# Kernel tuning notes

Measured on AMD Instinct MI355X. Metric: run time of the kernel, lower is better.

The kernel has to match this reference:

```python
import jax, jax.numpy as jnp
import numpy as np

BATCH, D_INNER, DT_RANK, N = 256, 5120, 160, 16

def _softplus_thresh(z, threshold=20.0):
    # softplus(z) with beta=1; linear above threshold (matches ttnn.softplus(parameter1=1, parameter2=20))
    return jnp.where(z > threshold, z, jax.nn.softplus(z))

def setup_inputs() -> dict:
    key = jax.random.key(0)
    ks = jax.random.split(key, 9)
    s = lambda d: 1.0 / np.sqrt(d)
    return {
        "x": jax.random.normal(ks[0], (1, 1, BATCH, D_INNER), jnp.float32),
        "h": jax.random.normal(ks[1], (BATCH, D_INNER, N), jnp.float32) * 0.1,
        "W_delta": jax.random.normal(ks[2], (D_INNER, DT_RANK), jnp.float32) * s(D_INNER),
        "W_dt": jax.random.normal(ks[3], (DT_RANK, D_INNER), jnp.float32) * s(DT_RANK),
        "b_dt": jax.random.normal(ks[4], (D_INNER,), jnp.float32) * 0.1,
        "A_log": jax.random.uniform(ks[5], (D_INNER, N), jnp.float32, 0.0, 1.5),
        "W_B": jax.random.normal(ks[6], (D_INNER, N), jnp.float32) * s(D_INNER),
        "W_C": jax.random.normal(ks[7], (D_INNER, N), jnp.float32) * s(D_INNER),
        "D": jax.random.normal(ks[8], (D_INNER,), jnp.float32),
    }

def reference(x, h, W_delta, W_dt, b_dt, A_log, W_B, W_C, D):
    # x: (1,1,B,d_inner) single decode step; h: (B,d_inner,n) SSM state
    xb = x.reshape(BATCH, D_INNER)                           # (B, d)
    # delta = softplus(x @ W_delta @ W_dt + b_dt)           -> (B, d)
    dt = _softplus_thresh((xb @ W_delta) @ W_dt + b_dt)
    A = -jnp.exp(A_log)                                      # (d, n)
    abar = jnp.exp(dt[:, :, None] * A[None, :, :])           # (B, d, n)
    Bp = xb @ W_B                                            # (B, n)
    # bbar * x: delta * B * x, broadcast over state dim
    bx = (dt * xb)[:, :, None] * Bp[:, None, :]              # (B, d, n)
    h_new = abar * h + bx                                    # (B, d, n) new hidden state
    C = xb @ W_C                                             # (B, n)
    y = jnp.einsum("bdn,bn->bd", h_new, C) + xb * D          # readout + skip (D)
    return y.reshape(1, 1, BATCH, D_INNER)
```

## Files before the change

### kernel.cpp

```cpp
#include <hip/hip_runtime.h>
#include <math.h>

#define BATCH 256
#define DIN   5120
#define RANK  160
#define NS    16
#define NCAT  192

__global__ __launch_bounds__(256) void k1_gemm(
    const float* __restrict__ x, const float* __restrict__ Wd,
    const float* __restrict__ WB, const float* __restrict__ WC,
    float* __restrict__ P, float* __restrict__ Bp, float* __restrict__ Cc)
{
    __shared__ float xT[32][64];
    __shared__ float Wt[32][64];
    const int t  = threadIdx.x;
    const int m0 = blockIdx.x * 64;
    const int n0 = blockIdx.y * 64;
    const int k0 = blockIdx.z * 128;
    const int tm = (t >> 4) * 4;
    const int tn = (t & 15) * 4;

    const int lm  = t >> 2;
    const int lk  = (t & 3) * 8;
    const int ln  = t & 63;
    const int lkb = (t >> 6) * 8;

    const float* wsrc; int wstr;
    {
        const int c = n0 + ln;
        if (c < RANK)            { wsrc = Wd + c;                wstr = RANK; }
        else if (c < RANK + NS)  { wsrc = WB + (c - RANK);       wstr = NS;   }
        else                     { wsrc = WC + (c - RANK - NS);  wstr = NS;   }
    }

    float acc[4][4] = {{0.f}};

    for (int ks = 0; ks < 4; ++ks) {
        const int kb = k0 + ks * 32;
        {
            const float* src = x + (size_t)(m0 + lm) * DIN + kb + lk;
            const float4 a0 = *(const float4*)src;
            const float4 a1 = *(const float4*)(src + 4);
            xT[lk+0][lm]=a0.x; xT[lk+1][lm]=a0.y; xT[lk+2][lm]=a0.z; xT[lk+3][lm]=a0.w;
            xT[lk+4][lm]=a1.x; xT[lk+5][lm]=a1.y; xT[lk+6][lm]=a1.z; xT[lk+7][lm]=a1.w;
        }
        {
            const float* wp = wsrc + (size_t)(kb + lkb) * wstr;
            #pragma unroll
            for (int i = 0; i < 8; ++i) { Wt[lkb + i][ln] = *wp; wp += wstr; }
        }
        __syncthreads();
        #pragma unroll
        for (int k = 0; k < 32; ++k) {
            const float4 a = *(const float4*)&xT[k][tm];
            const float4 b = *(const float4*)&Wt[k][tn];
            acc[0][0] += a.x*b.x; acc[0][1] += a.x*b.y; acc[0][2] += a.x*b.z; acc[0][3] += a.x*b.w;
            acc[1][0] += a.y*b.x; acc[1][1] += a.y*b.y; acc[1][2] += a.y*b.z; acc[1][3] += a.y*b.w;
            acc[2][0] += a.z*b.x; acc[2][1] += a.z*b.y; acc[2][2] += a.z*b.z; acc[2][3] += a.z*b.w;
            acc[3][0] += a.w*b.x; acc[3][1] += a.w*b.y; acc[3][2] += a.w*b.z; acc[3][3] += a.w*b.w;
        }
        __syncthreads();
    }

    #pragma unroll
    for (int i = 0; i < 4; ++i) {
        const int gm = m0 + tm + i;
        #pragma unroll
        for (int j = 0; j < 4; ++j) {
            const int c = n0 + tn + j;
            float* dst;
            if (c < RANK)           dst = P  + gm * RANK + c;
            else if (c < RANK + NS) dst = Bp + gm * NS + (c - RANK);
            else                    dst = Cc + gm * NS + (c - RANK - NS);
            atomicAdd(dst, acc[i][j]);
        }
    }
}

__device__ __forceinline__ float softplus20(float z)
{
    if (z > 20.f) return z;
    return fmaxf(z, 0.f) + log1pf(__expf(-fabsf(z)));
}

__global__ __launch_bounds__(256) void k2a_gemm(
    const float* __restrict__ P, const float* __restrict__ Wdt,
    const float* __restrict__ bdt, float* __restrict__ dtb)
{
    __shared__ float aT[32][64];
    __shared__ float Bt[32][64];
    const int t  = threadIdx.x;
    const int m0 = blockIdx.x * 64;
    const int n0 = blockIdx.y * 64;
    const int tm = (t >> 4) * 4;
    const int tn = (t & 15) * 4;

    const int lm  = t >> 2;
    const int lk  = (t & 3) * 8;
    const int ln  = t & 63;
    const int lkb = (t >> 6) * 8;

    float acc[4][4] = {{0.f}};

    for (int ks = 0; ks < 5; ++ks) {
        const int kb = ks * 32;
        {
            const float* src = P + (size_t)(m0 + lm) * RANK + kb + lk;
            const float4 a0 = *(const float4*)src;
            const float4 a1 = *(const float4*)(src + 4);
            aT[lk+0][lm]=a0.x; aT[lk+1][lm]=a0.y; aT[lk+2][lm]=a0.z; aT[lk+3][lm]=a0.w;
            aT[lk+4][lm]=a1.x; aT[lk+5][lm]=a1.y; aT[lk+6][lm]=a1.z; aT[lk+7][lm]=a1.w;
        }
        {
            const float* wp = Wdt + (size_t)(kb + lkb) * DIN + n0 + ln;
            #pragma unroll
            for (int i = 0; i < 8; ++i) { Bt[lkb + i][ln] = wp[(size_t)i * DIN]; }
        }
        __syncthreads();
        #pragma unroll
        for (int k = 0; k < 32; ++k) {
            const float4 a = *(const float4*)&aT[k][tm];
            const float4 b = *(const float4*)&Bt[k][tn];
            acc[0][0] += a.x*b.x; acc[0][1] += a.x*b.y; acc[0][2] += a.x*b.z; acc[0][3] += a.x*b.w;
            acc[1][0] += a.y*b.x; acc[1][1] += a.y*b.y; acc[1][2] += a.y*b.z; acc[1][3] += a.y*b.w;
            acc[2][0] += a.z*b.x; acc[2][1] += a.z*b.y; acc[2][2] += a.z*b.z; acc[2][3] += a.z*b.w;
            acc[3][0] += a.w*b.x; acc[3][1] += a.w*b.y; acc[3][2] += a.w*b.z; acc[3][3] += a.w*b.w;
        }
        __syncthreads();
    }

    const float4 bz = *(const float4*)&bdt[n0 + tn];
    #pragma unroll
    for (int i = 0; i < 4; ++i) {
        const int gm = m0 + tm + i;
        float4 o;
        o.x = softplus20(acc[i][0] + bz.x);
        o.y = softplus20(acc[i][1] + bz.y);
        o.z = softplus20(acc[i][2] + bz.z);
        o.w = softplus20(acc[i][3] + bz.w);
        *(float4*)&dtb[(size_t)gm * DIN + n0 + tn] = o;
    }
}

__global__ __launch_bounds__(256) void k2b_ssm(
    const float* __restrict__ dtb, const float* __restrict__ x,
    const float* __restrict__ h, const float* __restrict__ A_log,
    const float* __restrict__ Bp, const float* __restrict__ Cc,
    const float* __restrict__ Dv, float* __restrict__ y)
{
    __shared__ float sB[4][NS];
    __shared__ float sC[4][NS];

    const int tid = threadIdx.x;
    const int d   = blockIdx.x * 256 + tid;
    const int b0  = blockIdx.y * 4;

    if (tid < 64)                    sB[tid >> 4][tid & 15] = Bp[b0 * NS + tid];
    else if (tid < 128) { int u = tid - 64; sC[u >> 4][u & 15] = Cc[b0 * NS + u]; }
    __syncthreads();

    float A2[NS];
    {
        const float4* ap = (const float4*)(A_log + (size_t)d * NS);
        #pragma unroll
        for (int q = 0; q < 4; ++q) {
            const float4 a4 = ap[q];
            A2[4*q+0] = -1.442695041f * __expf(a4.x);
            A2[4*q+1] = -1.442695041f * __expf(a4.y);
            A2[4*q+2] = -1.442695041f * __expf(a4.z);
            A2[4*q+3] = -1.442695041f * __expf(a4.w);
        }
    }
    const float dv = Dv[d];

    #pragma unroll
    for (int b = 0; b < 4; ++b) {
        const int gb = b0 + b;
        const float dtv = dtb[(size_t)gb * DIN + d];
        const float xv  = x[(size_t)gb * DIN + d];
        const float dtx = dtv * xv;
        const float4* hp = (const float4*)(h + ((size_t)gb * DIN + d) * NS);
        float s = 0.f;
        #pragma unroll
        for (int q = 0; q < 4; ++q) {
            const float4 h4 = hp[q];
            s += (exp2f(dtv * A2[4*q+0]) * h4.x + dtx * sB[b][4*q+0]) * sC[b][4*q+0];
            s += (exp2f(dtv * A2[4*q+1]) * h4.y + dtx * sB[b][4*q+1]) * sC[b][4*q+1];
            s += (exp2f(dtv * A2[4*q+2]) * h4.z + dtx * sB[b][4*q+2]) * sC[b][4*q+2];
            s += (exp2f(dtv * A2[4*q+3]) * h4.w + dtx * sB[b][4*q+3]) * sC[b][4*q+3];
        }
        y[(size_t)gb * DIN + d] = s + xv * dv;
    }
}

extern "C" void kernel_launch(void* const* d_in, const int* in_sizes, int n_in,
                              void* d_out, int out_size, void* d_ws, size_t ws_size,
                              hipStream_t stream)
{
    const float* x     = (const float*)d_in[0];
    const float* h     = (const float*)d_in[1];
    const float* Wd    = (const float*)d_in[2];
    const float* Wdt   = (const float*)d_in[3];
    const float* bdt   = (const float*)d_in[4];
    const float* A_log = (const float*)d_in[5];
    const float* WB    = (const float*)d_in[6];
    const float* WC    = (const float*)d_in[7];
    const float* Dv    = (const float*)d_in[8];
    float* out = (float*)d_out;

    float* ws  = (float*)d_ws;
    float* P   = ws;
    float* Bp  = ws + BATCH * RANK;
    float* Cc  = Bp + BATCH * NS;
    float* dtb = Cc + BATCH * NS;

    hipMemsetAsync(ws, 0, (size_t)BATCH * NCAT * sizeof(float), stream);

    k1_gemm <<<dim3(4, 3, 40), 256, 0, stream>>>(x, Wd, WB, WC, P, Bp, Cc);
    k2a_gemm<<<dim3(4, 80),    256, 0, stream>>>(P, Wdt, bdt, dtb);
    k2b_ssm <<<dim3(20, 64),   256, 0, stream>>>(dtb, x, h, A_log, Bp, Cc, Dv, out);
}
```

Measured before the change: 205.4 us.

## Fuse three kernels into one persistent kernel with software grid barriers

Merges the x-projection GEMM, the dt GEMM with softplus, and the SSM readout into one kernel launched with 480 blocks, separated by atomic-counter grid barriers. The SSM phase becomes a grid-stride loop over the original 1280 tiles. The intent is to remove the launch gaps and tail effects between the three kernels. It relies on all 480 blocks being co-resident, otherwise the spin barriers deadlock. The barriers themselves add spin-wait cost, and fewer blocks in the memory-bound SSM phase may lower achieved bandwidth.

```diff
diff --git a/kernel.cpp b/kernel.cpp
--- a/kernel.cpp
+++ b/kernel.cpp
@@ -6,76 +6,17 @@
 #define RANK  160
 #define NS    16
 #define NCAT  192
-
-__global__ __launch_bounds__(256) void k1_gemm(
-    const float* __restrict__ x, const float* __restrict__ Wd,
-    const float* __restrict__ WB, const float* __restrict__ WC,
-    float* __restrict__ P, float* __restrict__ Bp, float* __restrict__ Cc)
-{
-    __shared__ float xT[32][64];
-    __shared__ float Wt[32][64];
-    const int t  = threadIdx.x;
-    const int m0 = blockIdx.x * 64;
-    const int n0 = blockIdx.y * 64;
-    const int k0 = blockIdx.z * 128;
-    const int tm = (t >> 4) * 4;
-    const int tn = (t & 15) * 4;
-
-    const int lm  = t >> 2;
-    const int lk  = (t & 3) * 8;
-    const int ln  = t & 63;
-    const int lkb = (t >> 6) * 8;
-
-    const float* wsrc; int wstr;
-    {
-        const int c = n0 + ln;
-        if (c < RANK)            { wsrc = Wd + c;                wstr = RANK; }
-        else if (c < RANK + NS)  { wsrc = WB + (c - RANK);       wstr = NS;   }
-        else                     { wsrc = WC + (c - RANK - NS);  wstr = NS;   }
-    }
-
-    float acc[4][4] = {{0.f}};
-
-    for (int ks = 0; ks < 4; ++ks) {
-        const int kb = k0 + ks * 32;
-        {
-            const float* src = x + (size_t)(m0 + lm) * DIN + kb + lk;
-            const float4 a0 = *(const float4*)src;
-            const float4 a1 = *(const float4*)(src + 4);
-            xT[lk+0][lm]=a0.x; xT[lk+1][lm]=a0.y; xT[lk+2][lm]=a0.z; xT[lk+3][lm]=a0.w;
-            xT[lk+4][lm]=a1.x; xT[lk+5][lm]=a1.y; xT[lk+6][lm]=a1.z; xT[lk+7][lm]=a1.w;
-        }
-        {
-            const float* wp = wsrc + (size_t)(kb + lkb) * wstr;
-            #pragma unroll
-            for (int i = 0; i < 8; ++i) { Wt[lkb + i][ln] = *wp; wp += wstr; }
-        }
-        __syncthreads();
-        #pragma unroll
-        for (int k = 0; k < 32; ++k) {
-            const float4 a = *(const float4*)&xT[k][tm];
-            const float4 b = *(const float4*)&Wt[k][tn];
-            acc[0][0] += a.x*b.x; acc[0][1] += a.x*b.y; acc[0][2] += a.x*b.z; acc[0][3] += a.x*b.w;
-            acc[1][0] += a.y*b.x; acc[1][1] += a.y*b.y; acc[1][2] += a.y*b.z; acc[1][3] += a.y*b.w;
-            acc[2][0] += a.z*b.x; acc[2][1] += a.z*b.y; acc[2][2] += a.z*b.z; acc[2][3] += a.z*b.w;
-            acc[3][0] += a.w*b.x; acc[3][1] += a.w*b.y; acc[3][2] += a.w*b.z; acc[3][3] += a.w*b.w;
-        }
-        __syncthreads();
-    }
-
-    #pragma unroll
-    for (int i = 0; i < 4; ++i) {
-        const int gm = m0 + tm + i;
-        #pragma unroll
-        for (int j = 0; j < 4; ++j) {
-            const int c = n0 + tn + j;
-            float* dst;
-            if (c < RANK)           dst = P  + gm * RANK + c;
-            else if (c < RANK + NS) dst = Bp + gm * NS + (c - RANK);
-            else                    dst = Cc + gm * NS + (c - RANK - NS);
-            atomicAdd(dst, acc[i][j]);
-        }
-    }
+#define GRID  480
+
+__device__ __forceinline__ void grid_barrier(int* ctr, int nblk)
+{
+    __syncthreads();
+    if (threadIdx.x == 0) {
+        __hip_atomic_fetch_add(ctr, 1, __ATOMIC_RELEASE, __HIP_MEMORY_SCOPE_AGENT);
+        while (__hip_atomic_load(ctr, __ATOMIC_ACQUIRE, __HIP_MEMORY_SCOPE_AGENT) < nblk)
+            __builtin_amdgcn_s_sleep(2);
+    }
+    __syncthreads();
 }
 
 __device__ __forceinline__ float softplus20(float z)
@@ -84,113 +25,184 @@
     return fmaxf(z, 0.f) + log1pf(__expf(-fabsf(z)));
 }
 
-__global__ __launch_bounds__(256) void k2a_gemm(
-    const float* __restrict__ P, const float* __restrict__ Wdt,
-    const float* __restrict__ bdt, float* __restrict__ dtb)
-{
-    __shared__ float aT[32][64];
-    __shared__ float Bt[32][64];
-    const int t  = threadIdx.x;
-    const int m0 = blockIdx.x * 64;
-    const int n0 = blockIdx.y * 64;
-    const int tm = (t >> 4) * 4;
-    const int tn = (t & 15) * 4;
-
-    const int lm  = t >> 2;
-    const int lk  = (t & 3) * 8;
-    const int ln  = t & 63;
-    const int lkb = (t >> 6) * 8;
-
-    float acc[4][4] = {{0.f}};
-
-    for (int ks = 0; ks < 5; ++ks) {
-        const int kb = ks * 32;
+__global__ __launch_bounds__(256) void mega(
+    const float* __restrict__ x, const float* __restrict__ h,
+    const float* __restrict__ Wd, const float* __restrict__ Wdt,
+    const float* __restrict__ bdt, const float* __restrict__ A_log,
+    const float* __restrict__ WB, const float* __restrict__ WC,
+    const float* __restrict__ Dv,
+    int* __restrict__ bar, float* __restrict__ P,
+    float* __restrict__ Bp, float* __restrict__ Cc,
+    float* __restrict__ dtb, float* __restrict__ y)
+{
+    __shared__ float sA[32][64];
+    __shared__ float sW[32][64];
+    __shared__ float sB4[4][NS];
+    __shared__ float sC4[4][NS];
+
+    const int t   = threadIdx.x;
+    const int blk = blockIdx.x;
+
+    {
+        const int m0 = (blk & 3) * 64;
+        const int n0 = ((blk >> 2) % 3) * 64;
+        const int k0 = (blk / 12) * 128;
+        const int tm = (t >> 4) * 4;
+        const int tn = (t & 15) * 4;
+        const int lm  = t >> 2;
+        const int lk  = (t & 3) * 8;
+        const int ln  = t & 63;
+        const int lkb = (t >> 6) * 8;
+
+        const float* wsrc; int wstr;
         {
-            const float* src = P + (size_t)(m0 + lm) * RANK + kb + lk;
-            const float4 a0 = *(const float4*)src;
-            const float4 a1 = *(const float4*)(src + 4);
-            aT[lk+0][lm]=a0.x; aT[lk+1][lm]=a0.y; aT[lk+2][lm]=a0.z; aT[lk+3][lm]=a0.w;
-            aT[lk+4][lm]=a1.x; aT[lk+5][lm]=a1.y; aT[lk+6][lm]=a1.z; aT[lk+7][lm]=a1.w;
-        }
+            const int c = n0 + ln;
+            if (c < RANK)            { wsrc = Wd + c;                wstr = RANK; }
+            else if (c < RANK + NS)  { wsrc = WB + (c - RANK);       wstr = NS;   }
+            else                     { wsrc = WC + (c - RANK - NS);  wstr = NS;   }
+        }
+
+        float acc[4][4] = {{0.f}};
+
+        for (int ks = 0; ks < 4; ++ks) {
+            const int kb = k0 + ks * 32;
+            {
+                const float* src = x + (size_t)(m0 + lm) * DIN + kb + lk;
+                const float4 a0 = *(const float4*)src;
+                const float4 a1 = *(const float4*)(src + 4);
+                sA[lk+0][lm]=a0.x; sA[lk+1][lm]=a0.y; sA[lk+2][lm]=a0.z; sA[lk+3][lm]=a0.w;
+                sA[lk+4][lm]=a1.x; sA[lk+5][lm]=a1.y; sA[lk+6][lm]=a1.z; sA[lk+7][lm]=a1.w;
+            }
+            {
+                const float* wp = wsrc + (size_t)(kb + lkb) * wstr;
+                #pragma unroll
+                for (int i = 0; i < 8; ++i) { sW[lkb + i][ln] = *wp; wp += wstr; }
+            }
+            __syncthreads();
+            #pragma unroll
+            for (int k = 0; k < 32; ++k) {
+                const float4 a = *(const float4*)&sA[k][tm];
+                const float4 b = *(const float4*)&sW[k][tn];
+                acc[0][0] += a.x*b.x; acc[0][1] += a.x*b.y; acc[0][2] += a.x*b.z; acc[0][3] += a.x*b.w;
+                acc[1][0] += a.y*b.x; acc[1][1] += a.y*b.y; acc[1][2] += a.y*b.z; acc[1][3] += a.y*b.w;
+                acc[2][0] += a.z*b.x; acc[2][1] += a.z*b.y; acc[2][2] += a.z*b.z; acc[2][3] += a.z*b.w;
+                acc[3][0] += a.w*b.x; acc[3][1] += a.w*b.y; acc[3][2] += a.w*b.z; acc[3][3] += a.w*b.w;
+            }
+            __syncthreads();
+        }
+
+        #pragma unroll
+        for (int i = 0; i < 4; ++i) {
+            const int gm = m0 + tm + i;
+            #pragma unroll
+            for (int j = 0; j < 4; ++j) {
+                const int c = n0 + tn + j;
+                float* dst;
+                if (c < RANK)           dst = P  + gm * RANK + c;
+                else if (c < RANK + NS) dst = Bp + gm * NS + (c - RANK);
+                else                    dst = Cc + gm * NS + (c - RANK - NS);
+                atomicAdd(dst, acc[i][j]);
+            }
+        }
+    }
+
+    grid_barrier(&bar[0], GRID);
+
+    if (blk < 320) {
+        const int m0 = (blk & 3) * 64;
+        const int n0 = (blk >> 2) * 64;
+        const int tm = (t >> 4) * 4;
+        const int tn = (t & 15) * 4;
+        const int lm  = t >> 2;
+        const int lk  = (t & 3) * 8;
+        const int ln  = t & 63;
+        const int lkb = (t >> 6) * 8;
+
+        float acc[4][4] = {{0.f}};
+
+        for (int ks = 0; ks < 5; ++ks) {
+            const int kb = ks * 32;
+            {
+                const float* src = P + (size_t)(m0 + lm) * RANK + kb + lk;
+                const float4 a0 = *(const float4*)src;
+                const float4 a1 = *(const float4*)(src + 4);
+                sA[lk+0][lm]=a0.x; sA[lk+1][lm]=a0.y; sA[lk+2][lm]=a0.z; sA[lk+3][lm]=a0.w;
+                sA[lk+4][lm]=a1.x; sA[lk+5][lm]=a1.y; sA[lk+6][lm]=a1.z; sA[lk+7][lm]=a1.w;
+            }
+            {
+                const float* wp = Wdt + (size_t)(kb + lkb) * DIN + n0 + ln;
+                #pragma unroll
+                for (int i = 0; i < 8; ++i) { sW[lkb + i][ln] = wp[(size_t)i * DIN]; }
+            }
+            __syncthreads();
+            #pragma unroll
+            for (int k = 0; k < 32; ++k) {
+                const float4 a = *(const float4*)&sA[k][tm];
+                const float4 b = *(const float4*)&sW[k][tn];
+                acc[0][0] += a.x*b.x; acc[0][1] += a.x*b.y; acc[0][2] += a.x*b.z; acc[0][3] += a.x*b.w;
+                acc[1][0] += a.y*b.x; acc[1][1] += a.y*b.y; acc[1][2] += a.y*b.z; acc[1][3] += a.y*b.w;
+                acc[2][0] += a.z*b.x; acc[2][1] += a.z*b.y; acc[2][2] += a.z*b.z; acc[2][3] += a.z*b.w;
+                acc[3][0] += a.w*b.x; acc[3][1] += a.w*b.y; acc[3][2] += a.w*b.z; acc[3][3] += a.w*b.w;
+            }
+            __syncthreads();
+        }
+
+        const float4 bz = *(const float4*)&bdt[n0 + tn];
+        #pragma unroll
+        for (int i = 0; i < 4; ++i) {
+            const int gm = m0 + tm + i;
+            float4 o;
+            o.x = softplus20(acc[i][0] + bz.x);
+            o.y = softplus20(acc[i][1] + bz.y);
+            o.z = softplus20(acc[i][2] + bz.z);
+            o.w = softplus20(acc[i][3] + bz.w);
+            *(float4*)&dtb[(size_t)gm * DIN + n0 + tn] = o;
+        }
+    }
+
+    grid_barrier(&bar[1], GRID);
+
+    for (int vb = blk; vb < 1280; vb += GRID) {
+        const int d  = (vb % 20) * 256 + t;
+        const int b0 = (vb / 20) * 4;
+
+        __syncthreads();
+        if (t < 64)                    sB4[t >> 4][t & 15] = Bp[b0 * NS + t];
+        else if (t < 128) { int u = t - 64; sC4[u >> 4][u & 15] = Cc[b0 * NS + u]; }
+        __syncthreads();
+
+        float A2[NS];
         {
-            const float* wp = Wdt + (size_t)(kb + lkb) * DIN + n0 + ln;
-            #pragma unroll
-            for (int i = 0; i < 8; ++i) { Bt[lkb + i][ln] = wp[(size_t)i * DIN]; }
-        }
-        __syncthreads();
+            const float4* ap = (const float4*)(A_log + (size_t)d * NS);
+            #pragma unroll
+            for (int q = 0; q < 4; ++q) {
+                const float4 a4 = ap[q];
+                A2[4*q+0] = -1.442695041f * __expf(a4.x);
+                A2[4*q+1] = -1.442695041f * __expf(a4.y);
+                A2[4*q+2] = -1.442695041f * __expf(a4.z);
+                A2[4*q+3] = -1.442695041f * __expf(a4.w);
+            }
+        }
+        const float dv = Dv[d];
+
         #pragma unroll
-        for (int k = 0; k < 32; ++k) {
-            const float4 a = *(const float4*)&aT[k][tm];
-            const float4 b = *(const float4*)&Bt[k][tn];
-            acc[0][0] += a.x*b.x; acc[0][1] += a.x*b.y; acc[0][2] += a.x*b.z; acc[0][3] += a.x*b.w;
-            acc[1][0] += a.y*b.x; acc[1][1] += a.y*b.y; acc[1][2] += a.y*b.z; acc[1][3] += a.y*b.w;
-            acc[2][0] += a.z*b.x; acc[2][1] += a.z*b.y; acc[2][2] += a.z*b.z; acc[2][3] += a.z*b.w;
-            acc[3][0] += a.w*b.x; acc[3][1] += a.w*b.y; acc[3][2] += a.w*b.z; acc[3][3] += a.w*b.w;
-        }
-        __syncthreads();
-    }
-
-    const float4 bz = *(const float4*)&bdt[n0 + tn];
-    #pragma unroll
-    for (int i = 0; i < 4; ++i) {
-        const int gm = m0 + tm + i;
-        float4 o;
-        o.x = softplus20(acc[i][0] + bz.x);
-        o.y = softplus20(acc[i][1] + bz.y);
-        o.z = softplus20(acc[i][2] + bz.z);
-        o.w = softplus20(acc[i][3] + bz.w);
-        *(float4*)&dtb[(size_t)gm * DIN + n0 + tn] = o;
-    }
-}
-
-__global__ __launch_bounds__(256) void k2b_ssm(
-    const float* __restrict__ dtb, const float* __restrict__ x,
-    const float* __restrict__ h, const float* __restrict__ A_log,
-    const float* __restrict__ Bp, const float* __restrict__ Cc,
-    const float* __restrict__ Dv, float* __restrict__ y)
-{
-    __shared__ float sB[4][NS];
-    __shared__ float sC[4][NS];
-
-    const int tid = threadIdx.x;
-    const int d   = blockIdx.x * 256 + tid;
-    const int b0  = blockIdx.y * 4;
-
-    if (tid < 64)                    sB[tid >> 4][tid & 15] = Bp[b0 * NS + tid];
-    else if (tid < 128) { int u = tid - 64; sC[u >> 4][u & 15] = Cc[b0 * NS + u]; }
-    __syncthreads();
-
-    float A2[NS];
-    {
-        const float4* ap = (const float4*)(A_log + (size_t)d * NS);
-        #pragma unroll
-        for (int q = 0; q < 4; ++q) {
-            const float4 a4 = ap[q];
-            A2[4*q+0] = -1.442695041f * __expf(a4.x);
-            A2[4*q+1] = -1.442695041f * __expf(a4.y);
-            A2[4*q+2] = -1.442695041f * __expf(a4.z);
-            A2[4*q+3] = -1.442695041f * __expf(a4.w);
-        }
-    }
-    const float dv = Dv[d];
-
-    #pragma unroll
-    for (int b = 0; b < 4; ++b) {
-        const int gb = b0 + b;
-        const float dtv = dtb[(size_t)gb * DIN + d];
-        const float xv  = x[(size_t)gb * DIN + d];
-        const float dtx = dtv * xv;
-        const float4* hp = (const float4*)(h + ((size_t)gb * DIN + d) * NS);
-        float s = 0.f;
-        #pragma unroll
-        for (int q = 0; q < 4; ++q) {
-            const float4 h4 = hp[q];
-            s += (exp2f(dtv * A2[4*q+0]) * h4.x + dtx * sB[b][4*q+0]) * sC[b][4*q+0];
-            s += (exp2f(dtv * A2[4*q+1]) * h4.y + dtx * sB[b][4*q+1]) * sC[b][4*q+1];
-            s += (exp2f(dtv * A2[4*q+2]) * h4.z + dtx * sB[b][4*q+2]) * sC[b][4*q+2];
-            s += (exp2f(dtv * A2[4*q+3]) * h4.w + dtx * sB[b][4*q+3]) * sC[b][4*q+3];
-        }
-        y[(size_t)gb * DIN + d] = s + xv * dv;
+        for (int b = 0; b < 4; ++b) {
+            const int gb = b0 + b;
+            const float dtv = dtb[(size_t)gb * DIN + d];
+            const float xv  = x[(size_t)gb * DIN + d];
+            const float dtx = dtv * xv;
+            const float4* hp = (const float4*)(h + ((size_t)gb * DIN + d) * NS);
+            float s = 0.f;
+            #pragma unroll
+            for (int q = 0; q < 4; ++q) {
+                const float4 h4 = hp[q];
+                s += (exp2f(dtv * A2[4*q+0]) * h4.x + dtx * sB4[b][4*q+0]) * sC4[b][4*q+0];
+                s += (exp2f(dtv * A2[4*q+1]) * h4.y + dtx * sB4[b][4*q+1]) * sC4[b][4*q+1];
+                s += (exp2f(dtv * A2[4*q+2]) * h4.z + dtx * sB4[b][4*q+2]) * sC4[b][4*q+2];
+                s += (exp2f(dtv * A2[4*q+3]) * h4.w + dtx * sB4[b][4*q+3]) * sC4[b][4*q+3];
+            }
+            y[(size_t)gb * DIN + d] = s + xv * dv;
+        }
     }
 }
 
@@ -209,15 +221,14 @@
     const float* Dv    = (const float*)d_in[8];
     float* out = (float*)d_out;
 
-    float* ws  = (float*)d_ws;
-    float* P   = ws;
-    float* Bp  = ws + BATCH * RANK;
+    int*   bar = (int*)d_ws;
+    float* P   = (float*)d_ws + 16;
+    float* Bp  = P  + BATCH * RANK;
     float* Cc  = Bp + BATCH * NS;
     float* dtb = Cc + BATCH * NS;
 
-    hipMemsetAsync(ws, 0, (size_t)BATCH * NCAT * sizeof(float), stream);
-
-    k1_gemm <<<dim3(4, 3, 40), 256, 0, stream>>>(x, Wd, WB, WC, P, Bp, Cc);
-    k2a_gemm<<<dim3(4, 80),    256, 0, stream>>>(P, Wdt, bdt, dtb);
-    k2b_ssm <<<dim3(20, 64),   256, 0, stream>>>(dtb, x, h, A_log, Bp, Cc, Dv, out);
-}
+    hipMemsetAsync(d_ws, 0, (16 + (size_t)BATCH * NCAT) * sizeof(float), stream);
+
+    mega<<<dim3(GRID), 256, 0, stream>>>(x, h, Wd, Wdt, bdt, A_log, WB, WC, Dv,
+                                         bar, P, Bp, Cc, dtb, out);
+}
```

Result: slower. 301.0 us (+46.5%).

## Replace split-K atomics with partial-sum reduce and coalesce SSM state reads

Applied to the files above, without the earlier changes.

The first GEMM now writes per-split partial sums to a workspace buffer, and a separate reduce kernel sums them, replacing the memset plus scalar atomicAdds. The SSM kernel is restructured so each group of 4 lanes reads one contiguous 64-byte row of h with float4 loads and combines the results with wave shuffles, giving coalesced access to the large state tensor. In exchange it adds one kernel launch and about 7.8 MB of partial-sum traffic, and it recomputes exp(A_log) for every batch row instead of reusing it across 4.

```diff
diff --git a/kernel.cpp b/kernel.cpp
--- a/kernel.cpp
+++ b/kernel.cpp
@@ -6,18 +6,20 @@
 #define RANK  160
 #define NS    16
 #define NCAT  192
-
-__global__ __launch_bounds__(256) void k1_gemm(
+#define NSPLIT 40
+
+__global__ __launch_bounds__(256) void k1a_gemm(
     const float* __restrict__ x, const float* __restrict__ Wd,
     const float* __restrict__ WB, const float* __restrict__ WC,
-    float* __restrict__ P, float* __restrict__ Bp, float* __restrict__ Cc)
+    float* __restrict__ psum)
 {
     __shared__ float xT[32][64];
     __shared__ float Wt[32][64];
     const int t  = threadIdx.x;
     const int m0 = blockIdx.x * 64;
     const int n0 = blockIdx.y * 64;
-    const int k0 = blockIdx.z * 128;
+    const int z  = blockIdx.z;
+    const int k0 = z * 128;
     const int tm = (t >> 4) * 4;
     const int tn = (t & 15) * 4;
 
@@ -63,19 +65,28 @@
         __syncthreads();
     }
 
+    float* dst = psum + (size_t)z * (BATCH * NCAT);
     #pragma unroll
     for (int i = 0; i < 4; ++i) {
         const int gm = m0 + tm + i;
-        #pragma unroll
-        for (int j = 0; j < 4; ++j) {
-            const int c = n0 + tn + j;
-            float* dst;
-            if (c < RANK)           dst = P  + gm * RANK + c;
-            else if (c < RANK + NS) dst = Bp + gm * NS + (c - RANK);
-            else                    dst = Cc + gm * NS + (c - RANK - NS);
-            atomicAdd(dst, acc[i][j]);
-        }
-    }
+        float4 o; o.x = acc[i][0]; o.y = acc[i][1]; o.z = acc[i][2]; o.w = acc[i][3];
+        *(float4*)&dst[(size_t)gm * NCAT + n0 + tn] = o;
+    }
+}
+
+__global__ __launch_bounds__(256) void k1r_reduce(
+    const float* __restrict__ psum, float* __restrict__ P,
+    float* __restrict__ Bp, float* __restrict__ Cc)
+{
+    const int o = blockIdx.x * 256 + threadIdx.x;
+    float s = 0.f;
+    #pragma unroll 8
+    for (int z = 0; z < NSPLIT; ++z) s += psum[(size_t)z * (BATCH * NCAT) + o];
+    const int gm = o / NCAT;
+    const int gc = o - gm * NCAT;
+    if (gc < RANK)           P [gm * RANK + gc]             = s;
+    else if (gc < RANK + NS) Bp[gm * NS   + gc - RANK]      = s;
+    else                     Cc[gm * NS   + gc - RANK - NS] = s;
 }
 
 __device__ __forceinline__ float softplus20(float z)
@@ -143,54 +154,51 @@
     }
 }
 
-__global__ __launch_bounds__(256) void k2b_ssm(
+__global__ __launch_bounds__(256) void k3_ssm(
     const float* __restrict__ dtb, const float* __restrict__ x,
     const float* __restrict__ h, const float* __restrict__ A_log,
     const float* __restrict__ Bp, const float* __restrict__ Cc,
     const float* __restrict__ Dv, float* __restrict__ y)
 {
-    __shared__ float sB[4][NS];
-    __shared__ float sC[4][NS];
-
-    const int tid = threadIdx.x;
-    const int d   = blockIdx.x * 256 + tid;
-    const int b0  = blockIdx.y * 4;
-
-    if (tid < 64)                    sB[tid >> 4][tid & 15] = Bp[b0 * NS + tid];
-    else if (tid < 128) { int u = tid - 64; sC[u >> 4][u & 15] = Cc[b0 * NS + u]; }
-    __syncthreads();
-
-    float A2[NS];
-    {
-        const float4* ap = (const float4*)(A_log + (size_t)d * NS);
+    const int t    = threadIdx.x;
+    const int lane = t & 63;
+    const int wv   = t >> 6;
+    const int b    = blockIdx.x / 20;
+    const int d0   = (blockIdx.x % 20) * 256 + wv * 64;
+
+    const int v = lane & 3;
+    const int j = lane >> 2;
+
+    const float4 B4 = *(const float4*)(Bp + b * NS + v * 4);
+    const float4 C4 = *(const float4*)(Cc + b * NS + v * 4);
+
+    float res[4];
+    #pragma unroll
+    for (int q = 0; q < 4; ++q) {
+        const int c = d0 + q * 16 + j;
+        const float dtv = dtb[(size_t)b * DIN + c];
+        const float xv  = x  [(size_t)b * DIN + c];
+        const float dtx = dtv * xv;
+        const float4 h4 = *(const float4*)(h     + ((size_t)b * DIN + c) * NS + v * 4);
+        const float4 a4 = *(const float4*)(A_log + (size_t)c * NS + v * 4);
+        float s;
+        s  = (exp2f(dtv * (-1.442695041f * __expf(a4.x))) * h4.x + dtx * B4.x) * C4.x;
+        s += (exp2f(dtv * (-1.442695041f * __expf(a4.y))) * h4.y + dtx * B4.y) * C4.y;
+        s += (exp2f(dtv * (-1.442695041f * __expf(a4.z))) * h4.z + dtx * B4.z) * C4.z;
+        s += (exp2f(dtv * (-1.442695041f * __expf(a4.w))) * h4.w + dtx * B4.w) * C4.w;
+        if (v == 0) s += xv * Dv[c];
+        res[q] = s;
+    }
+
+    #pragma unroll
+    for (int q = 0; q < 4; ++q) {
+        res[q] += __shfl_xor(res[q], 1, 64);
+        res[q] += __shfl_xor(res[q], 2, 64);
+    }
+    if (v == 0) {
         #pragma unroll
-        for (int q = 0; q < 4; ++q) {
-            const float4 a4 = ap[q];
-            A2[4*q+0] = -1.442695041f * __expf(a4.x);
-            A2[4*q+1] = -1.442695041f * __expf(a4.y);
-            A2[4*q+2] = -1.442695041f * __expf(a4.z);
-            A2[4*q+3] = -1.442695041f * __expf(a4.w);
-        }
-    }
-    const float dv = Dv[d];
-
-    #pragma unroll
-    for (int b = 0; b < 4; ++b) {
-        const int gb = b0 + b;
-        const float dtv = dtb[(size_t)gb * DIN + d];
-        const float xv  = x[(size_t)gb * DIN + d];
-        const float dtx = dtv * xv;
-        const float4* hp = (const float4*)(h + ((size_t)gb * DIN + d) * NS);
-        float s = 0.f;
-        #pragma unroll
-        for (int q = 0; q < 4; ++q) {
-            const float4 h4 = hp[q];
-            s += (exp2f(dtv * A2[4*q+0]) * h4.x + dtx * sB[b][4*q+0]) * sC[b][4*q+0];
-            s += (exp2f(dtv * A2[4*q+1]) * h4.y + dtx * sB[b][4*q+1]) * sC[b][4*q+1];
-            s += (exp2f(dtv * A2[4*q+2]) * h4.z + dtx * sB[b][4*q+2]) * sC[b][4*q+2];
-            s += (exp2f(dtv * A2[4*q+3]) * h4.w + dtx * sB[b][4*q+3]) * sC[b][4*q+3];
-        }
-        y[(size_t)gb * DIN + d] = s + xv * dv;
+        for (int q = 0; q < 4; ++q)
+            y[(size_t)b * DIN + d0 + q * 16 + j] = res[q];
     }
 }
 
@@ -209,15 +217,14 @@
     const float* Dv    = (const float*)d_in[8];
     float* out = (float*)d_out;
 
-    float* ws  = (float*)d_ws;
-    float* P   = ws;
-    float* Bp  = ws + BATCH * RANK;
-    float* Cc  = Bp + BATCH * NS;
-    float* dtb = Cc + BATCH * NS;
-
-    hipMemsetAsync(ws, 0, (size_t)BATCH * NCAT * sizeof(float), stream);
-
-    k1_gemm <<<dim3(4, 3, 40), 256, 0, stream>>>(x, Wd, WB, WC, P, Bp, Cc);
-    k2a_gemm<<<dim3(4, 80),    256, 0, stream>>>(P, Wdt, bdt, dtb);
-    k2b_ssm <<<dim3(20, 64),   256, 0, stream>>>(dtb, x, h, A_log, Bp, Cc, Dv, out);
-}
+    float* psum = (float*)d_ws;
+    float* P    = psum + (size_t)NSPLIT * BATCH * NCAT;
+    float* Bp   = P  + BATCH * RANK;
+    float* Cc   = Bp + BATCH * NS;
+    float* dtb  = Cc + BATCH * NS;
+
+    k1a_gemm  <<<dim3(4, 3, NSPLIT), 256, 0, stream>>>(x, Wd, WB, WC, psum);
+    k1r_reduce<<<dim3(NCAT),         256, 0, stream>>>(psum, P, Bp, Cc);
+    k2a_gemm  <<<dim3(4, 80),        256, 0, stream>>>(P, Wdt, bdt, dtb);
+    k3_ssm    <<<dim3(BATCH * 20),   256, 0, stream>>>(dtb, x, h, A_log, Bp, Cc, Dv, out);
+}
```

Result: faster. 182.2 us (-11.3%).
